# Performance work log

Measured on AMD Instinct MI355X. Metric: run time of the kernel, lower is better.

The kernel has to match this reference:

```python
import jax, jax.numpy as jnp
import numpy as np

N, M, B = 2048, 2048, 1
D, H, DQK, DV = 1024, 16, 64, 64
OFFSET = 0
PARAM_SCALE = 0.02  # keeps logits in a sane range (original uses plain randn)


def setup_inputs() -> dict:
    key = jax.random.key(0)
    ks = jax.random.split(key, 7)
    return {
        "x_q": jax.random.normal(ks[0], (N, B, D), jnp.float32),
        "x_kv": jax.random.normal(ks[1], (M, B, D), jnp.float32),
        "to_q": jax.random.normal(ks[2], (DQK, H, D), jnp.float32) * PARAM_SCALE,
        "to_k": jax.random.normal(ks[3], (DQK, H, D), jnp.float32) * PARAM_SCALE,
        "to_v": jax.random.normal(ks[4], (DV, H, D), jnp.float32) * PARAM_SCALE,
        "to_out": jax.random.normal(ks[5], (D, DV, H), jnp.float32) * PARAM_SCALE,
        "for_pos_enc": jax.random.normal(ks[6], (DQK, H, D), jnp.float32) * PARAM_SCALE,
    }


def _sincos(n, m, offset, d_x_kv, dtype):
    # relative distances i - j + offset range over [offset-(m-1), offset+(n-1)]
    r = jnp.arange(offset - (m - 1), offset + (n - 1) + 1, dtype=dtype)  # [R], R=n+m-1
    inv_freq = 1.0 / (10000.0 ** (jnp.arange(0.0, d_x_kv, 2.0, dtype=dtype) / d_x_kv))
    phases = r[:, None] * inv_freq[None, :]  # [R, d/2]
    return jnp.concatenate([jnp.sin(phases), jnp.cos(phases)], axis=-1)  # [R, d]


def reference(x_q, x_kv, to_q, to_k, to_v, to_out, for_pos_enc):
    n, b, _ = x_q.shape
    m = x_kv.shape[0]
    # q: [n, d_qk, b, h]
    q = jnp.einsum('dhb,nab->ndah', to_q, x_q)
    # content logits: [n, m, b, h]
    k = jnp.einsum('dhc,mac->mdah', to_k, x_kv)
    content = jnp.einsum('ndah,mdah->nmah', q, k)
    # relative positional encoding (same math as pos_enc[dists - min] then einsum,
    # but logits computed per relative position then gathered -> no [n,m,d,h] blowup)
    sincos = _sincos(n, m, OFFSET, x_kv.shape[-1], x_q.dtype)  # [R, d_x_kv]
    pe_rel = jnp.einsum('dhb,rb->rdh', for_pos_enc, sincos)    # [R, d_qk, h]
    pl_rel = jnp.einsum('ndah,rdh->nrah', q, pe_rel)            # [n, R, b, h]
    idx = jnp.arange(n)[:, None] - jnp.arange(m)[None, :] + (m - 1)  # dists - dists.min()
    position = pl_rel[jnp.arange(n)[:, None], idx]               # [n, m, b, h]
    logits = content + position
    # causal mask: True above diagonal shifted by 1+offset
    mask = jnp.triu(jnp.ones((n, m), bool), 1 + OFFSET)
    logits = jnp.where(mask[:, :, None, None], -jnp.inf, logits)
    weights = jax.nn.softmax(logits, axis=1)                     # softmax over m
    v = jnp.einsum('chb,mab->mach', to_v, x_kv)                  # [m, b, dv, h]
    ctx = jnp.einsum('nmah,mach->nach', weights, v)              # [n, b, dv, h]
    out = jnp.einsum('dch,nach->nad', to_out, ctx)               # [n, b, d]
    return out
```

## Files before the change

### kernel.cpp

```cpp
#include <hip/hip_runtime.h>
#include <hip/hip_bf16.h>

#define N_Q   2048
#define M_KV  2048
#define DIM   1024
#define NH    16
#define DHEAD 64
#define KDIM  1024
#define PEROWS 2112
#define PEBUF  2176

typedef __attribute__((ext_vector_type(8))) __bf16 bf16x8;
typedef __attribute__((ext_vector_type(4))) float  f32x4;

typedef __attribute__((address_space(1))) const unsigned char gbyte_t;
typedef __attribute__((address_space(3))) unsigned char lbyte_t;

__device__ __forceinline__ unsigned short f2bf(float f) {
  union { float f; unsigned u; } v; v.f = f;
  unsigned u = v.u;
  u = u + 0x7fffu + ((u >> 16) & 1u);
  return (unsigned short)(u >> 16);
}

#define PREP_A 524288
#define PREP_B 1048576
#define PREP_C 2097152
#define PREP_D 2359296
#define PREP_E 2916352
__global__ __launch_bounds__(256) void prep_kernel(
    const float* __restrict__ x_q, const float* __restrict__ x_kv,
    const float* __restrict__ to_q, const float* __restrict__ to_k,
    const float* __restrict__ to_v, const float* __restrict__ to_pe,
    const float* __restrict__ to_out,
    unsigned short* __restrict__ xq_bf, unsigned short* __restrict__ xkv_bf,
    unsigned short* __restrict__ wq_bf, unsigned short* __restrict__ wkv_bf,
    unsigned short* __restrict__ wp_bf, unsigned short* __restrict__ wo_bf,
    unsigned short* __restrict__ sc_bf) {
  int gid = blockIdx.x * 256 + threadIdx.x;
  if (gid < PREP_B) {
    const float* src = (gid < PREP_A) ? x_q : x_kv;
    unsigned short* dst = (gid < PREP_A) ? xq_bf : xkv_bf;
    int e4 = (gid < PREP_A ? gid : gid - PREP_A) * 4;
    float4 v = *(const float4*)(src + e4);
    ushort4 o = { f2bf(v.x), f2bf(v.y), f2bf(v.z), f2bf(v.w) };
    *(ushort4*)(dst + e4) = o;
  } else if (gid < PREP_C) {
    int e = gid - PREP_B;
    int which = e >> 18, inner = e & 262143;
    int e4 = inner * 4;
    int j = e4 >> 10, b = e4 & 1023;
    int d = j & 63, h = j >> 6;
    const float* w = (which == 0) ? to_q : (which == 1) ? to_k : (which == 2) ? to_v : to_pe;
    unsigned short* o = (which == 0) ? wq_bf : (which == 1) ? wkv_bf
                       : (which == 2) ? (wkv_bf + (size_t)DIM * DIM) : wp_bf;
    float4 v = *(const float4*)(w + (size_t)(d * NH + h) * DIM + b);
    ushort4 u = { f2bf(v.x), f2bf(v.y), f2bf(v.z), f2bf(v.w) };
    *(ushort4*)(o + e4) = u;
  } else if (gid < PREP_D) {
    int e4 = (gid - PREP_C) * 4;
    int dd = e4 >> 10, jc = e4 & 1023;
    int c = jc & 63, h = jc >> 6;
    const float* base = to_out + (size_t)(dd * DHEAD + c) * NH + h;
    ushort4 u = { f2bf(base[0]), f2bf(base[16]), f2bf(base[32]), f2bf(base[48]) };
    *(ushort4*)(wo_bf + e4) = u;
  } else if (gid < PREP_E) {
    int e = gid - PREP_D;
    int r = e >> 8, t8 = e & 255;
    float ph0base = (float)(r - 63);
    unsigned short ss[2], cc[2];
    #pragma unroll
    for (int i = 0; i < 2; ++i) {
      int k2 = t8 * 2 + i;
      float invf = __expf((float)k2 * (-9.210340371976184f / 512.0f));
      float s, c;
      __sincosf(ph0base * invf, &s, &c);
      ss[i] = f2bf(s); cc[i] = f2bf(c);
    }
    unsigned short* row = sc_bf + (size_t)r * DIM;
    *(unsigned int*)(row + t8 * 2)       = (unsigned)ss[0] | ((unsigned)ss[1] << 16);
    *(unsigned int*)(row + t8 * 2 + 512) = (unsigned)cc[0] | ((unsigned)cc[1] << 16);
  }
}

__global__ __launch_bounds__(256) void gemm_in_kernel(
    const unsigned short* __restrict__ xq, const unsigned short* __restrict__ xkv,
    const unsigned short* __restrict__ sc,
    const unsigned short* __restrict__ wq, const unsigned short* __restrict__ wkv,
    const unsigned short* __restrict__ wp,
    unsigned short* __restrict__ qout, unsigned short* __restrict__ kout,
    unsigned short* __restrict__ vtout, unsigned short* __restrict__ peout) {
  int bid0 = (int)blockIdx.x;
  int bid  = (bid0 & 7) * 130 + (bid0 >> 3);
  const unsigned short *A, *B; unsigned short *C1, *C2;
  int Mr, maxBrow, mode, ax, by;
  if (bid < 256)      { int t = bid;       ax = t & 15; by = t >> 4; A = xq;  B = wq;  C1 = qout;  C2 = nullptr; Mr = N_Q;    maxBrow = DIM - 1;     mode = 1; }
  else if (bid < 768) { int t = bid - 256; ax = t & 15; by = t >> 4; A = xkv; B = wkv; C1 = kout;  C2 = vtout;   Mr = M_KV;   maxBrow = 2 * DIM - 1; mode = 3; }
  else                { int t = bid - 768; ax = t % 17; by = t / 17; A = sc;  B = wp;  C1 = peout; C2 = nullptr; Mr = PEROWS; maxBrow = DIM - 1;     mode = 1; }

  __shared__ unsigned short As[2][128][64];
  __shared__ unsigned short Bs[2][64][64];
  int tid  = threadIdx.x;
  int wave = tid >> 6, lane = tid & 63;
  int g = lane >> 4, r16 = lane & 15;
  int arow0 = ax * 128;
  int brow0 = by * 64;
  int amax  = Mr - 1;

  auto stage = [&](int buf, int kt) {
    #pragma unroll
    for (int n = 0; n < 4; ++n) {
      int seg  = wave * 4 + n;
      int rloc = seg * 8 + (lane >> 3);
      int cbyte = ((lane & 7) << 4) ^ ((rloc & 7) << 4);
      int grow = min(arow0 + rloc, amax);
      const unsigned short* gp = A + (size_t)grow * KDIM + kt + (cbyte >> 1);
      __builtin_amdgcn_global_load_lds((gbyte_t*)(const void*)gp,
                                       (lbyte_t*)(void*)&As[buf][seg * 8][0], 16, 0, 0);
    }
    #pragma unroll
    for (int n = 0; n < 2; ++n) {
      int seg  = wave * 2 + n;
      int rloc = seg * 8 + (lane >> 3);
      int cbyte = ((lane & 7) << 4) ^ ((rloc & 7) << 4);
      int grow = min(brow0 + rloc, maxBrow);
      const unsigned short* gp = B + (size_t)grow * KDIM + kt + (cbyte >> 1);
      __builtin_amdgcn_global_load_lds((gbyte_t*)(const void*)gp,
                                       (lbyte_t*)(void*)&Bs[buf][seg * 8][0], 16, 0, 0);
    }
  };

  f32x4 acc[2][4];
  #pragma unroll
  for (int i = 0; i < 2; ++i)
    #pragma unroll
    for (int j = 0; j < 4; ++j) acc[i][j] = (f32x4){0,0,0,0};

  stage(0, 0);
  asm volatile("s_waitcnt vmcnt(0)" ::: "memory");
  __syncthreads();

  int buf = 0;
  for (int t = 0; t < 16; ++t) {
    if (t < 15) stage(buf ^ 1, (t + 1) * 64);

    bf16x8 af[2][2], bfr[4][2];
    #pragma unroll
    for (int i = 0; i < 2; ++i)
      #pragma unroll
      for (int kk = 0; kk < 2; ++kk) {
        int r = wave * 32 + i * 16 + r16;
        int cb = ((kk << 6) | (g << 4)) ^ ((r & 7) << 4);
        af[i][kk] = *(const bf16x8*)((const char*)&As[buf][r][0] + cb);
      }
    #pragma unroll
    for (int j = 0; j < 4; ++j)
      #pragma unroll
      for (int kk = 0; kk < 2; ++kk) {
        int r = j * 16 + r16;
        int cb = ((kk << 6) | (g << 4)) ^ ((r & 7) << 4);
        bfr[j][kk] = *(const bf16x8*)((const char*)&Bs[buf][r][0] + cb);
      }
    __builtin_amdgcn_s_setprio(1);
    #pragma unroll
    for (int kk = 0; kk < 2; ++kk)
      #pragma unroll
      for (int i = 0; i < 2; ++i)
        #pragma unroll
        for (int j = 0; j < 4; ++j)
          acc[i][j] = __builtin_amdgcn_mfma_f32_16x16x32_bf16(af[i][kk], bfr[j][kk], acc[i][j], 0, 0, 0);
    __builtin_amdgcn_s_setprio(0);

    if (t < 15) {
      asm volatile("s_waitcnt vmcnt(0)" ::: "memory");
      __syncthreads();
      buf ^= 1;
    }
  }

  #pragma unroll
  for (int i = 0; i < 2; ++i)
    #pragma unroll
    for (int j = 0; j < 4; ++j)
      #pragma unroll
      for (int rr = 0; rr < 4; ++rr) {
        int row = arow0 + wave * 32 + i * 16 + g * 4 + rr;
        int col = brow0 + j * 16 + r16;
        float v = acc[i][j][rr];
        if (mode == 1) {
          if (row < Mr) C1[(size_t)row * 1024 + col] = f2bf(v);
        } else {
          if (col < 1024) C1[(size_t)row * 1024 + col] = f2bf(v);
          else            C2[(size_t)(col - 1024) * M_KV + row] = f2bf(v);
        }
      }
}

__global__ __launch_bounds__(256) void gemm_out_kernel(
    const unsigned short* __restrict__ A, const unsigned short* __restrict__ B,
    float* __restrict__ C1) {
  __shared__ unsigned short As[2][64][64];
  __shared__ unsigned short Bs[2][64][64];
  int tid  = threadIdx.x;
  int wave = tid >> 6, lane = tid & 63;
  int wr = wave >> 1, wc = wave & 1;
  int g = lane >> 4, r16 = lane & 15;
  int arow0 = blockIdx.x * 64;
  int brow0 = blockIdx.y * 64;

  auto stage = [&](int buf, int kt) {
    #pragma unroll
    for (int n = 0; n < 2; ++n) {
      int seg  = wave * 2 + n;
      int rloc = seg * 8 + (lane >> 3);
      int cbyte = ((lane & 7) << 4) ^ ((rloc & 7) << 4);
      const unsigned short* gpA = A + (size_t)(arow0 + rloc) * KDIM + kt + (cbyte >> 1);
      __builtin_amdgcn_global_load_lds((gbyte_t*)(const void*)gpA,
                                       (lbyte_t*)(void*)&As[buf][seg * 8][0], 16, 0, 0);
      const unsigned short* gpB = B + (size_t)(brow0 + rloc) * KDIM + kt + (cbyte >> 1);
      __builtin_amdgcn_global_load_lds((gbyte_t*)(const void*)gpB,
                                       (lbyte_t*)(void*)&Bs[buf][seg * 8][0], 16, 0, 0);
    }
  };

  f32x4 acc[2][2] = {{{0,0,0,0},{0,0,0,0}},{{0,0,0,0},{0,0,0,0}}};

  stage(0, 0);
  asm volatile("s_waitcnt vmcnt(0)" ::: "memory");
  __syncthreads();

  int buf = 0;
  for (int t = 0; t < 16; ++t) {
    if (t < 15) stage(buf ^ 1, (t + 1) * 64);
    bf16x8 af[2][2], bfr[2][2];
    #pragma unroll
    for (int i = 0; i < 2; ++i)
      #pragma unroll
      for (int kk = 0; kk < 2; ++kk) {
        int r = wr * 32 + i * 16 + r16;
        int cb = ((kk << 6) | (g << 4)) ^ ((r & 7) << 4);
        af[i][kk] = *(const bf16x8*)((const char*)&As[buf][r][0] + cb);
      }
    #pragma unroll
    for (int j = 0; j < 2; ++j)
      #pragma unroll
      for (int kk = 0; kk < 2; ++kk) {
        int r = wc * 32 + j * 16 + r16;
        int cb = ((kk << 6) | (g << 4)) ^ ((r & 7) << 4);
        bfr[j][kk] = *(const bf16x8*)((const char*)&Bs[buf][r][0] + cb);
      }
    __builtin_amdgcn_s_setprio(1);
    #pragma unroll
    for (int kk = 0; kk < 2; ++kk)
      #pragma unroll
      for (int i = 0; i < 2; ++i)
        #pragma unroll
        for (int j = 0; j < 2; ++j)
          acc[i][j] = __builtin_amdgcn_mfma_f32_16x16x32_bf16(af[i][kk], bfr[j][kk], acc[i][j], 0, 0, 0);
    __builtin_amdgcn_s_setprio(0);
    if (t < 15) {
      asm volatile("s_waitcnt vmcnt(0)" ::: "memory");
      __syncthreads();
      buf ^= 1;
    }
  }

  #pragma unroll
  for (int i = 0; i < 2; ++i)
    #pragma unroll
    for (int j = 0; j < 2; ++j)
      #pragma unroll
      for (int rr = 0; rr < 4; ++rr) {
        int row = arow0 + wr * 32 + i * 16 + g * 4 + rr;
        int col = brow0 + wc * 32 + j * 16 + r16;
        C1[(size_t)row * 1024 + col] = acc[i][j][rr];
      }
}

__global__ __launch_bounds__(256, 2) void attn_mfma_kernel(
    const unsigned short* __restrict__ qb, const unsigned short* __restrict__ kb,
    const unsigned short* __restrict__ vt, const unsigned short* __restrict__ pe,
    unsigned short* __restrict__ ctx, float* __restrict__ part) {
  int ord  = (int)blockIdx.x;
  int h    = ord & 15;
  int widx = 79 - (ord >> 4);
  int b, c;
  if (widx < 8)       { b = widx;                                  c = 0; }
  else if (widx < 24) { int t2 = widx - 8;  b = 8  + (t2 >> 1);    c = t2 & 1; }
  else if (widx < 48) { int t2 = widx - 24; int q3 = t2 / 3; b = 16 + q3; c = t2 - 3 * q3; }
  else                { int t2 = widx - 48; b = 24 + (t2 >> 2);    c = t2 & 3; }
  int n0   = b * 64;
  int nc   = (b < 8) ? 1 : (b >> 3) + 1;
  int t0   = c * 8;
  int tend = min(t0 + 8, b + 1);

  int wave = threadIdx.x >> 6;
  int lane = threadIdx.x & 63;
  int g    = lane >> 4;
  int r16  = lane & 15;

  __shared__ unsigned short Ks[2][64][64];
  __shared__ unsigned short Vs[2][64][64];
  __shared__ unsigned short PEs[2][128][64];
  __shared__ unsigned short W_lds[4][16][72];

  const unsigned short* qrow = qb + (size_t)(n0 + wave * 16 + r16) * DIM + h * 64 + g * 8;
  bf16x8 aq0 = *(const bf16x8*)(qrow);
  bf16x8 aq1 = *(const bf16x8*)(qrow + 32);

  union { unsigned short u[8]; bf16x8 v; } one_u;
  #pragma unroll
  for (int i = 0; i < 8; ++i) one_u.u[i] = 0x3F80;
  bf16x8 ones = one_u.v;

  f32x4 acc[4] = {{0,0,0,0},{0,0,0,0},{0,0,0,0},{0,0,0,0}};
  f32x4 lacc = {0,0,0,0};

  auto stage = [&](int bufn, int tilen) {
    int m0n = tilen * 64;
    int prb = n0 - m0n;
    #pragma unroll
    for (int n = 0; n < 2; ++n) {
      int seg  = wave * 2 + n;
      int rloc = seg * 8 + (lane >> 3);
      int cbyte = ((lane & 7) << 4) ^ ((rloc & 7) << 4);
      const unsigned short* gpk = kb + (size_t)(m0n + rloc) * KDIM + h * 64 + (cbyte >> 1);
      __builtin_amdgcn_global_load_lds((gbyte_t*)(const void*)gpk,
                                       (lbyte_t*)(void*)&Ks[bufn][seg * 8][0], 16, 0, 0);
    }
    #pragma unroll
    for (int n = 0; n < 2; ++n) {
      int seg  = wave * 2 + n;
      int rloc = seg * 8 + (lane >> 3);
      int cbyte = ((lane & 7) << 4) ^ ((rloc & 7) << 4);
      const unsigned short* gpv = vt + (size_t)(h * 64 + rloc) * M_KV + m0n + (cbyte >> 1);
      __builtin_amdgcn_global_load_lds((gbyte_t*)(const void*)gpv,
                                       (lbyte_t*)(void*)&Vs[bufn][seg * 8][0], 16, 0, 0);
    }
    #pragma unroll
    for (int n = 0; n < 4; ++n) {
      int seg  = wave * 4 + n;
      int rloc = seg * 8 + (lane >> 3);
      int cbyte = ((lane & 7) << 4) ^ ((rloc & 7) << 4);
      const unsigned short* gpp = pe + (size_t)(prb + rloc) * KDIM + h * 64 + (cbyte >> 1);
      __builtin_amdgcn_global_load_lds((gbyte_t*)(const void*)gpp,
                                       (lbyte_t*)(void*)&PEs[bufn][seg * 8][0], 16, 0, 0);
    }
  };

  int srcl[4]; bool hi_sel[4];
  #pragma unroll
  for (int rr = 0; rr < 4; ++rr) {
    srcl[rr]   = (g << 4) | ((g * 4 + rr + 63 - r16) & 15);
    hi_sel[rr] = (g * 4 + rr) > r16;
  }
  int sw = (r16 & 7) << 4;

  stage(0, t0);
  asm volatile("s_waitcnt vmcnt(0)" ::: "memory");
  __syncthreads();

  int buf = 0;
  for (int tile = t0; tile < tend; ++tile) {
    int m0 = tile * 64;
    bool more = (tile + 1 < tend);
    if (more) stage(buf ^ 1, tile + 1);

    f32x4 s[4];
    __builtin_amdgcn_s_setprio(1);
    #pragma unroll
    for (int ct = 0; ct < 4; ++ct) {
      const char* kbase = (const char*)&Ks[buf][ct * 16 + r16][0];
      bf16x8 k0 = *(const bf16x8*)(kbase + (((g << 4)) ^ sw));
      bf16x8 k1 = *(const bf16x8*)(kbase + ((64 | (g << 4)) ^ sw));
      f32x4 z = {0,0,0,0};
      z = __builtin_amdgcn_mfma_f32_16x16x32_bf16(aq0, k0, z, 0, 0, 0);
      z = __builtin_amdgcn_mfma_f32_16x16x32_bf16(aq1, k1, z, 0, 0, 0);
      s[ct] = z;
    }
    __builtin_amdgcn_s_setprio(0);

    if (more) { asm volatile("s_waitcnt vmcnt(8)" ::: "memory"); }
    else      { asm volatile("s_waitcnt vmcnt(0)" ::: "memory"); }
    __builtin_amdgcn_s_barrier();
    __builtin_amdgcn_sched_barrier(0);

    f32x4 z2[5];
    __builtin_amdgcn_s_setprio(1);
    #pragma unroll
    for (int cp = 0; cp < 5; ++cp) {
      const char* pbase = (const char*)&PEs[buf][wave * 16 + cp * 16 + r16][0];
      bf16x8 p0 = *(const bf16x8*)(pbase + (((g << 4)) ^ sw));
      bf16x8 p1 = *(const bf16x8*)(pbase + ((64 | (g << 4)) ^ sw));
      f32x4 z = {0,0,0,0};
      z = __builtin_amdgcn_mfma_f32_16x16x32_bf16(aq0, p0, z, 0, 0, 0);
      z = __builtin_amdgcn_mfma_f32_16x16x32_bf16(aq1, p1, z, 0, 0, 0);
      z2[cp] = z;
    }
    __builtin_amdgcn_s_setprio(0);

    bool diag = (m0 == n0);
    #pragma unroll
    for (int ct = 0; ct < 4; ++ct) {
      #pragma unroll
      for (int rr = 0; rr < 4; ++rr) {
        float vhi = __shfl(z2[4 - ct][rr], srcl[rr], 64);
        float vlo = __shfl(z2[3 - ct][rr], srcl[rr], 64);
        float p   = hi_sel[rr] ? vhi : vlo;
        int il = g * 4 + rr;
        int it = wave * 16 + il;
        int jt = ct * 16 + r16;
        float val = s[ct][rr] + p;
        if (diag && jt > it) val = -1e30f;
        s[ct][rr] = __expf(val);
      }
    }

    #pragma unroll
    for (int ct = 0; ct < 4; ++ct)
      #pragma unroll
      for (int rr = 0; rr < 4; ++rr)
        W_lds[wave][g * 4 + rr][ct * 16 + r16] = f2bf(s[ct][rr]);
    bf16x8 aw0 = *(const bf16x8*)(&W_lds[wave][r16][g * 8]);
    bf16x8 aw1 = *(const bf16x8*)(&W_lds[wave][r16][g * 8 + 32]);

    __builtin_amdgcn_s_setprio(1);
    #pragma unroll
    for (int ct = 0; ct < 4; ++ct) {
      const char* vbase = (const char*)&Vs[buf][ct * 16 + r16][0];
      bf16x8 v0 = *(const bf16x8*)(vbase + (((g << 4)) ^ sw));
      bf16x8 v1 = *(const bf16x8*)(vbase + ((64 | (g << 4)) ^ sw));
      f32x4 a = acc[ct];
      a = __builtin_amdgcn_mfma_f32_16x16x32_bf16(aw0, v0, a, 0, 0, 0);
      a = __builtin_amdgcn_mfma_f32_16x16x32_bf16(aw1, v1, a, 0, 0, 0);
      acc[ct] = a;
    }
    lacc = __builtin_amdgcn_mfma_f32_16x16x32_bf16(aw0, ones, lacc, 0, 0, 0);
    lacc = __builtin_amdgcn_mfma_f32_16x16x32_bf16(aw1, ones, lacc, 0, 0, 0);
    __builtin_amdgcn_s_setprio(0);

    if (more) {
      asm volatile("s_waitcnt vmcnt(6)" ::: "memory");
      __builtin_amdgcn_s_barrier();
      __builtin_amdgcn_sched_barrier(0);
      buf ^= 1;
    }
  }

  if (nc == 1) {
    #pragma unroll
    for (int rr = 0; rr < 4; ++rr) {
      float inv = 1.0f / lacc[rr];
      #pragma unroll
      for (int ct = 0; ct < 4; ++ct) {
        int row = n0 + wave * 16 + g * 4 + rr;
        ctx[(size_t)row * DIM + h * 64 + ct * 16 + r16] = f2bf(acc[ct][rr] * inv);
      }
    }
  } else {
    float* slot = part + ((size_t)((b - 8) * 16 + h) * 4 + c) * (64 * 68);
    #pragma unroll
    for (int ct = 0; ct < 4; ++ct)
      #pragma unroll
      for (int rr = 0; rr < 4; ++rr) {
        int row = wave * 16 + g * 4 + rr;
        slot[row * 68 + ct * 16 + r16] = acc[ct][rr];
      }
    if (r16 == 0) {
      #pragma unroll
      for (int rr = 0; rr < 4; ++rr) {
        int row = wave * 16 + g * 4 + rr;
        slot[row * 68 + 64] = lacc[rr];
      }
    }
  }
}

__global__ __launch_bounds__(256) void combine_kernel(const float* __restrict__ part,
                                                      unsigned short* __restrict__ ctx) {
  int bb = blockIdx.x;
  int h  = blockIdx.y;
  int b  = bb + 8;
  int nc = (b >> 3) + 1;
  int t  = threadIdx.x;
  int row = t >> 2, q = t & 3;
  const float* base = part + ((size_t)(bb * 16 + h) * 4) * (64 * 68) + row * 68;
  float lstar = 0.0f;
  for (int c2 = 0; c2 < nc; ++c2) lstar += base[c2 * 4352 + 64];
  float inv = 1.0f / lstar;
  for (int cc = 0; cc < 16; ++cc) {
    int col = q * 16 + cc;
    float o = 0.0f;
    for (int c2 = 0; c2 < nc; ++c2) o += base[c2 * 4352 + col];
    ctx[(size_t)(b * 64 + row) * DIM + h * 64 + col] = f2bf(o * inv);
  }
}

extern "C" void kernel_launch(void* const* d_in, const int* in_sizes, int n_in,
                              void* d_out, int out_size, void* d_ws, size_t ws_size,
                              hipStream_t stream) {
  const float* x_q    = (const float*)d_in[0];
  const float* x_kv   = (const float*)d_in[1];
  const float* to_q   = (const float*)d_in[2];
  const float* to_k   = (const float*)d_in[3];
  const float* to_v   = (const float*)d_in[4];
  const float* to_out = (const float*)d_in[5];
  const float* to_pe  = (const float*)d_in[6];

  char* ws = (char*)d_ws;
  size_t off = 0;
  auto alloc = [&](size_t bytes) -> char* {
    char* p = ws + off;
    off += (bytes + 255) & ~(size_t)255;
    return p;
  };

  unsigned short* xq_bf  = (unsigned short*)alloc((size_t)N_Q  * DIM * 2);
  unsigned short* xkv_bf = (unsigned short*)alloc((size_t)M_KV * DIM * 2);
  unsigned short* wq_bf  = (unsigned short*)alloc((size_t)DIM * DIM * 2);
  unsigned short* wkv_bf = (unsigned short*)alloc((size_t)2 * DIM * DIM * 2);
  unsigned short* wp_bf  = (unsigned short*)alloc((size_t)DIM * DIM * 2);
  unsigned short* wo_bf  = (unsigned short*)alloc((size_t)DIM * DIM * 2);
  unsigned short* sc_bf  = (unsigned short*)alloc((size_t)PEBUF * DIM * 2);
  unsigned short* q_bf   = (unsigned short*)alloc((size_t)N_Q  * DIM * 2);
  unsigned short* k_bf   = (unsigned short*)alloc((size_t)M_KV * DIM * 2);
  unsigned short* vt_bf  = (unsigned short*)alloc((size_t)DIM * M_KV * 2);
  unsigned short* pe_bf  = (unsigned short*)alloc((size_t)PEBUF * DIM * 2);
  unsigned short* ctx_bf = (unsigned short*)alloc((size_t)N_Q * DIM * 2);
  float*          part   = (float*)alloc((size_t)24 * 16 * 4 * 64 * 68 * 4);

  prep_kernel<<<11392, 256, 0, stream>>>(x_q, x_kv, to_q, to_k, to_v, to_pe, to_out,
                                         xq_bf, xkv_bf, wq_bf, wkv_bf, wp_bf, wo_bf, sc_bf);

  gemm_in_kernel<<<1040, 256, 0, stream>>>(xq_bf, xkv_bf, sc_bf, wq_bf, wkv_bf, wp_bf,
                                           q_bf, k_bf, vt_bf, pe_bf);

  attn_mfma_kernel<<<1280, 256, 0, stream>>>(q_bf, k_bf, vt_bf, pe_bf, ctx_bf, part);
  combine_kernel<<<dim3(24, NH), 256, 0, stream>>>(part, ctx_bf);

  gemm_out_kernel<<<dim3(32, 16), 256, 0, stream>>>(ctx_bf, wo_bf, (float*)d_out);
}
```

Before: 136.8 us.

## Single-buffer V and PE tiles, prefetch K two tiles ahead, raise occupancy to 3

Drops double buffering for the V and positional-encoding LDS tiles and keeps only K double-buffered, with K prefetched two tiles ahead. V and PE for the next tile are now issued after the current tile's PV matmul, and fine-grained vmcnt waits are placed before the PE and V uses. The smaller LDS footprint lets launch bounds rise from 2 to 3 blocks per SM to improve latency hiding. The cost is that PE and V loads are now exposed within each iteration instead of overlapping a full tile of compute, and extra barriers are added.

```diff
diff --git a/kernel.cpp b/kernel.cpp
--- a/kernel.cpp
+++ b/kernel.cpp
@@ -277,7 +277,7 @@
       }
 }
 
-__global__ __launch_bounds__(256, 2) void attn_mfma_kernel(
+__global__ __launch_bounds__(256, 3) void attn_mfma_kernel(
     const unsigned short* __restrict__ qb, const unsigned short* __restrict__ kb,
     const unsigned short* __restrict__ vt, const unsigned short* __restrict__ pe,
     unsigned short* __restrict__ ctx, float* __restrict__ part) {
@@ -300,8 +300,8 @@
   int r16  = lane & 15;
 
   __shared__ unsigned short Ks[2][64][64];
-  __shared__ unsigned short Vs[2][64][64];
-  __shared__ unsigned short PEs[2][128][64];
+  __shared__ unsigned short Vs[64][64];
+  __shared__ unsigned short PEs[128][64];
   __shared__ unsigned short W_lds[4][16][72];
 
   const unsigned short* qrow = qb + (size_t)(n0 + wave * 16 + r16) * DIM + h * 64 + g * 8;
@@ -316,9 +316,32 @@
   f32x4 acc[4] = {{0,0,0,0},{0,0,0,0},{0,0,0,0},{0,0,0,0}};
   f32x4 lacc = {0,0,0,0};
 
-  auto stage = [&](int bufn, int tilen) {
+  auto stage_pe = [&](int tilen) {
+    int prb = n0 - tilen * 64;
+    #pragma unroll
+    for (int n = 0; n < 4; ++n) {
+      int seg  = wave * 4 + n;
+      int rloc = seg * 8 + (lane >> 3);
+      int cbyte = ((lane & 7) << 4) ^ ((rloc & 7) << 4);
+      const unsigned short* gpp = pe + (size_t)(prb + rloc) * KDIM + h * 64 + (cbyte >> 1);
+      __builtin_amdgcn_global_load_lds((gbyte_t*)(const void*)gpp,
+                                       (lbyte_t*)(void*)&PEs[seg * 8][0], 16, 0, 0);
+    }
+  };
+  auto stage_v = [&](int tilen) {
     int m0n = tilen * 64;
-    int prb = n0 - m0n;
+    #pragma unroll
+    for (int n = 0; n < 2; ++n) {
+      int seg  = wave * 2 + n;
+      int rloc = seg * 8 + (lane >> 3);
+      int cbyte = ((lane & 7) << 4) ^ ((rloc & 7) << 4);
+      const unsigned short* gpv = vt + (size_t)(h * 64 + rloc) * M_KV + m0n + (cbyte >> 1);
+      __builtin_amdgcn_global_load_lds((gbyte_t*)(const void*)gpv,
+                                       (lbyte_t*)(void*)&Vs[seg * 8][0], 16, 0, 0);
+    }
+  };
+  auto stage_k = [&](int kb_, int tilen) {
+    int m0n = tilen * 64;
     #pragma unroll
     for (int n = 0; n < 2; ++n) {
       int seg  = wave * 2 + n;
@@ -326,25 +349,7 @@
       int cbyte = ((lane & 7) << 4) ^ ((rloc & 7) << 4);
       const unsigned short* gpk = kb + (size_t)(m0n + rloc) * KDIM + h * 64 + (cbyte >> 1);
       __builtin_amdgcn_global_load_lds((gbyte_t*)(const void*)gpk,
-                                       (lbyte_t*)(void*)&Ks[bufn][seg * 8][0], 16, 0, 0);
-    }
-    #pragma unroll
-    for (int n = 0; n < 2; ++n) {
-      int seg  = wave * 2 + n;
-      int rloc = seg * 8 + (lane >> 3);
-      int cbyte = ((lane & 7) << 4) ^ ((rloc & 7) << 4);
-      const unsigned short* gpv = vt + (size_t)(h * 64 + rloc) * M_KV + m0n + (cbyte >> 1);
-      __builtin_amdgcn_global_load_lds((gbyte_t*)(const void*)gpv,
-                                       (lbyte_t*)(void*)&Vs[bufn][seg * 8][0], 16, 0, 0);
-    }
-    #pragma unroll
-    for (int n = 0; n < 4; ++n) {
-      int seg  = wave * 4 + n;
-      int rloc = seg * 8 + (lane >> 3);
-      int cbyte = ((lane & 7) << 4) ^ ((rloc & 7) << 4);
-      const unsigned short* gpp = pe + (size_t)(prb + rloc) * KDIM + h * 64 + (cbyte >> 1);
-      __builtin_amdgcn_global_load_lds((gbyte_t*)(const void*)gpp,
-                                       (lbyte_t*)(void*)&PEs[bufn][seg * 8][0], 16, 0, 0);
+                                       (lbyte_t*)(void*)&Ks[kb_][seg * 8][0], 16, 0, 0);
     }
   };
 
@@ -356,21 +361,28 @@
   }
   int sw = (r16 & 7) << 4;
 
-  stage(0, t0);
-  asm volatile("s_waitcnt vmcnt(0)" ::: "memory");
+  stage_pe(t0);
+  stage_v(t0);
+  stage_k(0, t0);
+  if (t0 + 1 < tend) {
+    stage_k(1, t0 + 1);
+    asm volatile("s_waitcnt vmcnt(2)" ::: "memory");
+  } else {
+    asm volatile("s_waitcnt vmcnt(0)" ::: "memory");
+  }
   __syncthreads();
 
-  int buf = 0;
+  int kbuf = 0;
   for (int tile = t0; tile < tend; ++tile) {
     int m0 = tile * 64;
-    bool more = (tile + 1 < tend);
-    if (more) stage(buf ^ 1, tile + 1);
+    bool more  = (tile + 1 < tend);
+    bool more2 = (tile + 2 < tend);
 
     f32x4 s[4];
     __builtin_amdgcn_s_setprio(1);
     #pragma unroll
     for (int ct = 0; ct < 4; ++ct) {
-      const char* kbase = (const char*)&Ks[buf][ct * 16 + r16][0];
+      const char* kbase = (const char*)&Ks[kbuf][ct * 16 + r16][0];
       bf16x8 k0 = *(const bf16x8*)(kbase + (((g << 4)) ^ sw));
       bf16x8 k1 = *(const bf16x8*)(kbase + ((64 | (g << 4)) ^ sw));
       f32x4 z = {0,0,0,0};
@@ -380,8 +392,8 @@
     }
     __builtin_amdgcn_s_setprio(0);
 
-    if (more) { asm volatile("s_waitcnt vmcnt(8)" ::: "memory"); }
-    else      { asm volatile("s_waitcnt vmcnt(0)" ::: "memory"); }
+    if (more) { asm volatile("s_waitcnt vmcnt(4)" ::: "memory"); }
+    else      { asm volatile("s_waitcnt vmcnt(2)" ::: "memory"); }
     __builtin_amdgcn_s_barrier();
     __builtin_amdgcn_sched_barrier(0);
 
@@ -389,7 +401,7 @@
     __builtin_amdgcn_s_setprio(1);
     #pragma unroll
     for (int cp = 0; cp < 5; ++cp) {
-      const char* pbase = (const char*)&PEs[buf][wave * 16 + cp * 16 + r16][0];
+      const char* pbase = (const char*)&PEs[wave * 16 + cp * 16 + r16][0];
       bf16x8 p0 = *(const bf16x8*)(pbase + (((g << 4)) ^ sw));
       bf16x8 p1 = *(const bf16x8*)(pbase + ((64 | (g << 4)) ^ sw));
       f32x4 z = {0,0,0,0};
@@ -424,10 +436,15 @@
     bf16x8 aw0 = *(const bf16x8*)(&W_lds[wave][r16][g * 8]);
     bf16x8 aw1 = *(const bf16x8*)(&W_lds[wave][r16][g * 8 + 32]);
 
+    if (more) { asm volatile("s_waitcnt vmcnt(2)" ::: "memory"); }
+    else      { asm volatile("s_waitcnt vmcnt(0)" ::: "memory"); }
+    __builtin_amdgcn_s_barrier();
+    __builtin_amdgcn_sched_barrier(0);
+
     __builtin_amdgcn_s_setprio(1);
     #pragma unroll
     for (int ct = 0; ct < 4; ++ct) {
-      const char* vbase = (const char*)&Vs[buf][ct * 16 + r16][0];
+      const char* vbase = (const char*)&Vs[ct * 16 + r16][0];
       bf16x8 v0 = *(const bf16x8*)(vbase + (((g << 4)) ^ sw));
       bf16x8 v1 = *(const bf16x8*)(vbase + ((64 | (g << 4)) ^ sw));
       f32x4 a = acc[ct];
@@ -440,10 +457,13 @@
     __builtin_amdgcn_s_setprio(0);
 
     if (more) {
-      asm volatile("s_waitcnt vmcnt(6)" ::: "memory");
+      asm volatile("s_waitcnt vmcnt(0)" ::: "memory");
       __builtin_amdgcn_s_barrier();
       __builtin_amdgcn_sched_barrier(0);
-      buf ^= 1;
+      stage_pe(tile + 1);
+      stage_v(tile + 1);
+      if (more2) stage_k(kbuf, tile + 2);
+      kbuf ^= 1;
     }
   }
 
```

Measured after the change: 133.7 us. 2.3% less time.
